# Kernel tuning notes

Measured on AMD Instinct MI355X. Metric: run time of the kernel, lower is better.

## Reference

```python
import jax, jax.numpy as jnp
import numpy as np

NUM_GRAPHS = 512
NODES_PER_GRAPH = 200  # == N_rois
EDGES_PER_GRAPH = 3200  # avg degree 16
N_ROIS = 200
HIDDEN = 64
OUT = 2


def setup_inputs() -> dict:
    key = jax.random.key(0)
    ks = jax.random.split(key, 7)
    N = NUM_GRAPHS * NODES_PER_GRAPH
    E = NUM_GRAPHS * EDGES_PER_GRAPH
    x = jax.random.normal(ks[0], (N, N_ROIS), dtype=jnp.float32)
    # edges sampled within each graph's node block
    base = jnp.repeat(jnp.arange(NUM_GRAPHS, dtype=jnp.int64) * NODES_PER_GRAPH, EDGES_PER_GRAPH)
    local = jax.random.randint(ks[1], (2, E), 0, NODES_PER_GRAPH, dtype=jnp.int64)
    edge_index = local + base[None, :]
    batch = jnp.arange(N, dtype=jnp.int64) // NODES_PER_GRAPH
    conv_w = jax.random.normal(ks[2], (N_ROIS, HIDDEN), dtype=jnp.float32) * 0.1
    conv_b = jax.random.normal(ks[3], (HIDDEN,), dtype=jnp.float32) * 0.1
    lin_w = jax.random.normal(ks[4], (HIDDEN, OUT), dtype=jnp.float32) * 0.1
    lin_b = jax.random.normal(ks[5], (OUT,), dtype=jnp.float32) * 0.1
    return {"x": x, "edge_index": edge_index, "batch": batch,
            "conv_w": conv_w, "conv_b": conv_b, "lin_w": lin_w, "lin_b": lin_b}


def reference(x, edge_index, batch, conv_w, conv_b, lin_w, lin_b):
    N = x.shape[0]
    # GCNConv: linear transform first (N_rois -> hidden), then normalized aggregation
    h = x @ conv_w  # [N, H]
    loops = jnp.arange(N, dtype=edge_index.dtype)
    src = jnp.concatenate([edge_index[0], loops])  # add self-loops (PyG default)
    dst = jnp.concatenate([edge_index[1], loops])
    deg = jax.ops.segment_sum(jnp.ones_like(dst, dtype=h.dtype), dst, num_segments=N)
    dinv = jnp.where(deg > 0, jax.lax.rsqrt(deg), jnp.zeros_like(deg))
    norm = dinv[src] * dinv[dst]  # D^-1/2 (A+I) D^-1/2 edge weights
    agg = jax.ops.segment_sum(h[src] * norm[:, None], dst, num_segments=N) + conv_b
    hr = jax.nn.relu(agg)
    x_pool = jax.ops.segment_max(hr, batch, num_segments=NUM_GRAPHS)  # [G, H]
    out = x_pool @ lin_w + lin_b  # [G, OUT]
    return out, x_pool
```

## Files before the change

kernel.cpp:

```cpp
#include <hip/hip_runtime.h>

#define NUM_GRAPHS 512
#define NPG 200
#define EPG 3200
#define NROIS 200
#define HID 64
#define OUTC 2
#define KPAD 224
#define THREADS 512
#define APITCH 232
#define HPITCH 232

typedef short v8s __attribute__((ext_vector_type(8)));
typedef float v4f __attribute__((ext_vector_type(4)));

__device__ __forceinline__ unsigned bf16_rne(float f) {
  unsigned u = __float_as_uint(f);
  return (u + 0x7fffu + ((u >> 16) & 1u)) >> 16;
}

__global__ void prep_w(const float* __restrict__ cw, short* __restrict__ ws) {
  int idx = blockIdx.x * 256 + threadIdx.x;
  if (idx >= HID * KPAD) return;
  int ch = idx / KPAD, k = idx - ch * KPAD;
  float f = (k < NROIS) ? cw[k * HID + ch] : 0.f;
  unsigned hi = bf16_rne(f);
  float lo = f - __uint_as_float(hi << 16);
  ws[ch * KPAD + k] = (short)hi;
  ws[HID * KPAD + ch * KPAD + k] = (short)(__float_as_uint(lo) >> 16);
}

struct __align__(16) Smem {
  unsigned char adj[208 * APITCH];
  unsigned short hpT[HID * HPITCH];
  float dinv[NPG];
  int cnt[NPG];
  int pool[HID];
};

__global__ __launch_bounds__(THREADS, 4)
void gcn_fused(const float* __restrict__ x,
               const int* __restrict__ ei,
               const short* __restrict__ wT,
               const float* __restrict__ cw,
               const float* __restrict__ cb,
               const float* __restrict__ lw,
               const float* __restrict__ lb,
               float* __restrict__ out,
               int Etot, int useWs) {
  __shared__ Smem s;
  const int g = blockIdx.x;
  const int tid = threadIdx.x;
  const int base = g * NPG;
  const int ebase = g * EPG;
  const int lane = tid & 63;
  const int w = __builtin_amdgcn_readfirstlane(tid >> 6);
  const int ml = tid & 15;
  const int q  = (tid >> 4) & 3;

  {
    uint4* z = (uint4*)&s;
    const uint4 z4 = {0u, 0u, 0u, 0u};
    #pragma unroll
    for (int i = 0; i < 10; ++i) {
      int idx = tid + i * THREADS;
      if (idx < (208 * APITCH + HID * HPITCH * 2) / 16) z[idx] = z4;
    }
    if (tid < NPG) s.cnt[tid] = 0;
    if (tid < HID) s.pool[tid] = 0;
  }
  __syncthreads();

  int esrc[7], edst[7];
  #pragma unroll
  for (int r = 0; r < 7; ++r) {
    int e = tid + r * THREADS;
    esrc[r] = -1; edst[r] = 0;
    if (e < EPG) {
      esrc[r] = ei[ebase + e] - base;
      edst[r] = ei[Etot + ebase + e] - base;
      atomicAdd(&s.cnt[edst[r]], 1);
    }
  }
  __syncthreads();

  if (w == 0) {
    if (lane < 50) {
      #pragma unroll
      for (int t = 0; t < 4; ++t) {
        int i = 4 * lane + t;
        s.dinv[i] = rsqrtf((float)(s.cnt[i] + 1));
      }
    }
  }

  {
    unsigned* adjW = (unsigned*)s.adj;
    #pragma unroll
    for (int r = 0; r < 7; ++r) {
      if (esrc[r] >= 0) {
        int idx = edst[r] * APITCH + esrc[r];
        atomicAdd(&adjW[idx >> 2], 1u << ((idx & 3) * 8));
      }
    }
    if (tid < NPG) {
      int idx = tid * APITCH + tid;
      atomicAdd(&adjW[idx >> 2], 1u << ((idx & 3) * 8));
    }
  }
  __syncthreads();

  {
    int mts[2];
    mts[0] = w;
    mts[1] = (w < 5) ? 8 + w : -1;

    v4f acc[2][4];
    #pragma unroll
    for (int a = 0; a < 2; ++a)
      #pragma unroll
      for (int b = 0; b < 4; ++b)
        acc[a][b] = (v4f){0.f, 0.f, 0.f, 0.f};

    for (int kt = 0; kt < 7; ++kt) {
      const int k0 = kt * 32 + q * 8;

      v8s bhi[4], blo[4];
      if (useWs) {
        #pragma unroll
        for (int nt = 0; nt < 4; ++nt) {
          const int ch = nt * 16 + ml;
          bhi[nt] = *(const v8s*)(wT + ch * KPAD + k0);
          blo[nt] = *(const v8s*)(wT + HID * KPAD + ch * KPAD + k0);
        }
      } else {
        const bool kok = (k0 < NROIS);
        #pragma unroll
        for (int nt = 0; nt < 4; ++nt) {
          #pragma unroll
          for (int i = 0; i < 8; ++i) {
            float f = kok ? cw[(k0 + i) * HID + nt * 16 + ml] : 0.f;
            unsigned hb = bf16_rne(f);
            float lo = f - __uint_as_float(hb << 16);
            bhi[nt][i] = (short)hb;
            blo[nt][i] = (short)(__float_as_uint(lo) >> 16);
          }
        }
      }

      #pragma unroll
      for (int mi = 0; mi < 2; ++mi) {
        if (mts[mi] >= 0) {
          const int row = mts[mi] * 16 + ml;
          v8s ahi, alo;
          if (k0 < NROIS && row < NPG) {
            const float* px = x + (size_t)(base + row) * NROIS + k0;
            const float4 f0 = *(const float4*)px;
            const float4 f1 = *(const float4*)(px + 4);
            const float ff[8] = {f0.x, f0.y, f0.z, f0.w, f1.x, f1.y, f1.z, f1.w};
            #pragma unroll
            for (int i = 0; i < 8; ++i) {
              unsigned u = __float_as_uint(ff[i]);
              unsigned hb = u >> 16;
              float lo = ff[i] - __uint_as_float(hb << 16);
              ahi[i] = (short)hb;
              alo[i] = (short)(__float_as_uint(lo) >> 16);
            }
          } else {
            #pragma unroll
            for (int i = 0; i < 8; ++i) { ahi[i] = 0; alo[i] = 0; }
          }
          #pragma unroll
          for (int nt = 0; nt < 4; ++nt) {
            acc[mi][nt] = __builtin_amdgcn_mfma_f32_16x16x32_bf16(ahi, blo[nt], acc[mi][nt], 0, 0, 0);
            acc[mi][nt] = __builtin_amdgcn_mfma_f32_16x16x32_bf16(alo, bhi[nt], acc[mi][nt], 0, 0, 0);
            acc[mi][nt] = __builtin_amdgcn_mfma_f32_16x16x32_bf16(ahi, bhi[nt], acc[mi][nt], 0, 0, 0);
          }
        }
      }
    }

    #pragma unroll
    for (int mi = 0; mi < 2; ++mi) {
      if (mts[mi] >= 0) {
        #pragma unroll
        for (int r = 0; r < 4; ++r) {
          const int row = mts[mi] * 16 + q * 4 + r;
          if (row < NPG) {
            const float dv = s.dinv[row];
            #pragma unroll
            for (int nt = 0; nt < 4; ++nt)
              s.hpT[(nt * 16 + ml) * HPITCH + row] =
                  (unsigned short)bf16_rne(dv * acc[mi][nt][r]);
          }
        }
      }
    }
  }
  __syncthreads();

  {
    int mts[2];
    mts[0] = w;
    mts[1] = (w < 5) ? 8 + w : -1;

    v4f acc2[2][4];
    #pragma unroll
    for (int a = 0; a < 2; ++a)
      #pragma unroll
      for (int b = 0; b < 4; ++b)
        acc2[a][b] = (v4f){0.f, 0.f, 0.f, 0.f};

    for (int kt = 0; kt < 7; ++kt) {
      const int k0 = kt * 32 + q * 8;

      v8s bf[4];
      #pragma unroll
      for (int nt = 0; nt < 4; ++nt)
        bf[nt] = *(const v8s*)&s.hpT[(nt * 16 + ml) * HPITCH + k0];

      #pragma unroll
      for (int mi = 0; mi < 2; ++mi) {
        if (mts[mi] >= 0) {
          const int row = mts[mi] * 16 + ml;
          const uint2 dd = *(const uint2*)&s.adj[row * APITCH + k0];
          v8s af;
          #pragma unroll
          for (int i = 0; i < 4; ++i) {
            af[i]     = (short)(__float_as_uint((float)((dd.x >> (8 * i)) & 0xffu)) >> 16);
            af[i + 4] = (short)(__float_as_uint((float)((dd.y >> (8 * i)) & 0xffu)) >> 16);
          }
          #pragma unroll
          for (int nt = 0; nt < 4; ++nt)
            acc2[mi][nt] = __builtin_amdgcn_mfma_f32_16x16x32_bf16(af, bf[nt], acc2[mi][nt], 0, 0, 0);
        }
      }
    }

    float cbv[4];
    #pragma unroll
    for (int nt = 0; nt < 4; ++nt) cbv[nt] = cb[nt * 16 + ml];
    float mx[4] = {0.f, 0.f, 0.f, 0.f};
    #pragma unroll
    for (int mi = 0; mi < 2; ++mi) {
      if (mts[mi] >= 0) {
        #pragma unroll
        for (int r = 0; r < 4; ++r) {
          const int row = mts[mi] * 16 + q * 4 + r;
          if (row < NPG) {
            const float dv = s.dinv[row];
            #pragma unroll
            for (int nt = 0; nt < 4; ++nt) {
              float v = fmaxf(fmaf(dv, acc2[mi][nt][r], cbv[nt]), 0.f);
              mx[nt] = fmaxf(mx[nt], v);
            }
          }
        }
      }
    }
    #pragma unroll
    for (int nt = 0; nt < 4; ++nt) {
      mx[nt] = fmaxf(mx[nt], __shfl_xor(mx[nt], 16));
      mx[nt] = fmaxf(mx[nt], __shfl_xor(mx[nt], 32));
    }
    if (q == 0 && (lane >> 5) == 0) {
      #pragma unroll
      for (int nt = 0; nt < 4; ++nt)
        atomicMax(&s.pool[nt * 16 + ml], __float_as_int(mx[nt]));
    }
  }
  __syncthreads();

  if (tid < HID) {
    const float xp = __int_as_float(s.pool[tid]);
    out[NUM_GRAPHS * OUTC + g * HID + tid] = xp;
    float p0 = xp * lw[tid * 2 + 0];
    float p1 = xp * lw[tid * 2 + 1];
    #pragma unroll
    for (int off = 32; off > 0; off >>= 1) {
      p0 += __shfl_down(p0, off);
      p1 += __shfl_down(p1, off);
    }
    if (tid == 0) {
      out[g * OUTC + 0] = p0 + lb[0];
      out[g * OUTC + 1] = p1 + lb[1];
    }
  }
}

extern "C" void kernel_launch(void* const* d_in, const int* in_sizes, int n_in,
                              void* d_out, int out_size, void* d_ws, size_t ws_size,
                              hipStream_t stream) {
  const float* x  = (const float*)d_in[0];
  const int*   ei = (const int*)d_in[1];
  const float* cw = (const float*)d_in[3];
  const float* cb = (const float*)d_in[4];
  const float* lw = (const float*)d_in[5];
  const float* lb = (const float*)d_in[6];
  const int Etot = in_sizes[1] / 2;

  const size_t wsNeeded = (size_t)2 * HID * KPAD * sizeof(short);
  const int useWs = (ws_size >= wsNeeded) ? 1 : 0;
  if (useWs) {
    prep_w<<<(HID * KPAD + 255) / 256, 256, 0, stream>>>(cw, (short*)d_ws);
  }
  gcn_fused<<<NUM_GRAPHS, THREADS, 0, stream>>>(x, ei, (const short*)d_ws, cw,
                                                cb, lw, lb, (float*)d_out, Etot, useWs);
}
```

Before: 164.0 us.

## Split fused GCN into separate dense GEMM kernel and per-graph aggregation kernel

Moves the x @ conv_w product out of the per-graph fused kernel into its own GEMM kernel over 64-node tiles. That kernel stages x as split bf16 hi/lo in LDS and reads a pre-swizzled weight image laid out in MFMA lane order. Its bf16 output goes to a global workspace in transposed layout, and the aggregation kernel scales it by dinv while loading. The aim is higher occupancy and better load balance for the GEMM stage, which in the fused kernel ran at one 512-thread block per graph. In exchange it adds an extra global round trip of the hidden features (about 6.5 MB) and another kernel launch. The old fused path is kept as a fallback for when the workspace is too small.

```diff
diff --git a/kernel.cpp b/kernel.cpp
--- a/kernel.cpp
+++ b/kernel.cpp
@@ -6,10 +6,11 @@
 #define NROIS 200
 #define HID 64
 #define OUTC 2
-#define KPAD 224
-#define THREADS 512
+#define NT (NUM_GRAPHS * NPG)
 #define APITCH 232
 #define HPITCH 232
+#define WIMG_ELEMS (7 * 4 * 2 * 64 * 8)
+#define WS_NEEDED ((size_t)WIMG_ELEMS * 2 + (size_t)HID * NT * 2)
 
 typedef short v8s __attribute__((ext_vector_type(8)));
 typedef float v4f __attribute__((ext_vector_type(4)));
@@ -19,36 +20,115 @@
   return (u + 0x7fffu + ((u >> 16) & 1u)) >> 16;
 }
 
-__global__ void prep_w(const float* __restrict__ cw, short* __restrict__ ws) {
+__global__ void prep_wimg(const float* __restrict__ cw, unsigned short* __restrict__ wimg) {
   int idx = blockIdx.x * 256 + threadIdx.x;
-  if (idx >= HID * KPAD) return;
-  int ch = idx / KPAD, k = idx - ch * KPAD;
+  if (idx >= WIMG_ELEMS) return;
+  int i    = idx & 7;
+  int lane = (idx >> 3) & 63;
+  int hl   = (idx >> 9) & 1;
+  int nt   = (idx >> 10) & 3;
+  int kt   = idx >> 12;
+  int k  = kt * 32 + (lane >> 4) * 8 + i;
+  int ch = nt * 16 + (lane & 15);
   float f = (k < NROIS) ? cw[k * HID + ch] : 0.f;
   unsigned hi = bf16_rne(f);
   float lo = f - __uint_as_float(hi << 16);
-  ws[ch * KPAD + k] = (short)hi;
-  ws[HID * KPAD + ch * KPAD + k] = (short)(__float_as_uint(lo) >> 16);
+  wimg[idx] = hl ? (unsigned short)(__float_as_uint(lo) >> 16) : (unsigned short)hi;
 }
 
-struct __align__(16) Smem {
+struct __align__(16) Smem1 {
+  unsigned short xhi[64 * HPITCH];
+  unsigned short xlo[64 * HPITCH];
+};
+
+__global__ __launch_bounds__(256, 2)
+void gcn_gemm1(const float* __restrict__ x,
+               const unsigned short* __restrict__ wimg,
+               unsigned short* __restrict__ hpT) {
+  __shared__ Smem1 s;
+  const int tid = threadIdx.x;
+  const int blk = blockIdx.x;
+  const int lane = tid & 63;
+  const int w = __builtin_amdgcn_readfirstlane(tid >> 6);
+  const int ml = tid & 15;
+  const int q  = (tid >> 4) & 3;
+
+  #pragma unroll
+  for (int t = 0; t < 13; ++t) {
+    int i = tid + t * 256;
+    if (i < 3200) {
+      int node = i / 50;
+      int kc = (i - node * 50) * 4;
+      const float4 v = *(const float4*)(x + (size_t)(blk * 64 + node) * NROIS + kc);
+      const float ff[4] = {v.x, v.y, v.z, v.w};
+      unsigned hh[4], ll[4];
+      #pragma unroll
+      for (int e = 0; e < 4; ++e) {
+        unsigned u = __float_as_uint(ff[e]);
+        hh[e] = u >> 16;
+        float lo = ff[e] - __uint_as_float(hh[e] << 16);
+        ll[e] = __float_as_uint(lo) >> 16;
+      }
+      uint2 ph = {hh[0] | (hh[1] << 16), hh[2] | (hh[3] << 16)};
+      uint2 pl = {ll[0] | (ll[1] << 16), ll[2] | (ll[3] << 16)};
+      *(uint2*)&s.xhi[node * HPITCH + kc] = ph;
+      *(uint2*)&s.xlo[node * HPITCH + kc] = pl;
+    }
+  }
+  for (int i = tid; i < 64 * 32; i += 256) {
+    int node = i >> 5, c = 200 + (i & 31);
+    s.xhi[node * HPITCH + c] = 0;
+    s.xlo[node * HPITCH + c] = 0;
+  }
+  __syncthreads();
+
+  v4f acc[4];
+  #pragma unroll
+  for (int nt = 0; nt < 4; ++nt) acc[nt] = (v4f){0.f, 0.f, 0.f, 0.f};
+
+  for (int kt = 0; kt < 7; ++kt) {
+    const int k0 = kt * 32 + q * 8;
+    const v8s xh = *(const v8s*)&s.xhi[(w * 16 + ml) * HPITCH + k0];
+    const v8s xl = *(const v8s*)&s.xlo[(w * 16 + ml) * HPITCH + k0];
+    #pragma unroll
+    for (int nt = 0; nt < 4; ++nt) {
+      const unsigned short* pw = wimg + (size_t)(((kt * 4 + nt) * 2) * 64 + lane) * 8;
+      const v8s whi = *(const v8s*)pw;
+      const v8s wlo = *(const v8s*)(pw + 64 * 8);
+      acc[nt] = __builtin_amdgcn_mfma_f32_16x16x32_bf16(whi, xl, acc[nt], 0, 0, 0);
+      acc[nt] = __builtin_amdgcn_mfma_f32_16x16x32_bf16(wlo, xh, acc[nt], 0, 0, 0);
+      acc[nt] = __builtin_amdgcn_mfma_f32_16x16x32_bf16(whi, xh, acc[nt], 0, 0, 0);
+    }
+  }
+
+  const int gnode = blk * 64 + w * 16 + ml;
+  #pragma unroll
+  for (int nt = 0; nt < 4; ++nt) {
+    #pragma unroll
+    for (int r = 0; r < 4; ++r) {
+      const int ch = nt * 16 + q * 4 + r;
+      hpT[(size_t)ch * NT + gnode] = (unsigned short)bf16_rne(acc[nt][r]);
+    }
+  }
+}
+
+struct __align__(16) Smem2 {
   unsigned char adj[208 * APITCH];
-  unsigned short hpT[HID * HPITCH];
+  unsigned short hpTl[HID * HPITCH];
   float dinv[NPG];
   int cnt[NPG];
   int pool[HID];
 };
 
-__global__ __launch_bounds__(THREADS, 4)
-void gcn_fused(const float* __restrict__ x,
-               const int* __restrict__ ei,
-               const short* __restrict__ wT,
-               const float* __restrict__ cw,
-               const float* __restrict__ cb,
-               const float* __restrict__ lw,
-               const float* __restrict__ lb,
-               float* __restrict__ out,
-               int Etot, int useWs) {
-  __shared__ Smem s;
+__global__ __launch_bounds__(512, 4)
+void gcn_agg(const int* __restrict__ ei,
+             const unsigned short* __restrict__ hpT,
+             const float* __restrict__ cb,
+             const float* __restrict__ lw,
+             const float* __restrict__ lb,
+             float* __restrict__ out,
+             int Etot) {
+  __shared__ Smem2 s;
   const int g = blockIdx.x;
   const int tid = threadIdx.x;
   const int base = g * NPG;
@@ -63,7 +143,7 @@
     const uint4 z4 = {0u, 0u, 0u, 0u};
     #pragma unroll
     for (int i = 0; i < 10; ++i) {
-      int idx = tid + i * THREADS;
+      int idx = tid + i * 512;
       if (idx < (208 * APITCH + HID * HPITCH * 2) / 16) z[idx] = z4;
     }
     if (tid < NPG) s.cnt[tid] = 0;
@@ -74,7 +154,7 @@
   int esrc[7], edst[7];
   #pragma unroll
   for (int r = 0; r < 7; ++r) {
-    int e = tid + r * THREADS;
+    int e = tid + r * 512;
     esrc[r] = -1; edst[r] = 0;
     if (e < EPG) {
       esrc[r] = ei[ebase + e] - base;
@@ -84,15 +164,8 @@
   }
   __syncthreads();
 
-  if (w == 0) {
-    if (lane < 50) {
-      #pragma unroll
-      for (int t = 0; t < 4; ++t) {
-        int i = 4 * lane + t;
-        s.dinv[i] = rsqrtf((float)(s.cnt[i] + 1));
-      }
-    }
-  }
+  if (tid < NPG) s.dinv[tid] = rsqrtf((float)(s.cnt[tid] + 1));
+  __syncthreads();
 
   {
     unsigned* adjW = (unsigned*)s.adj;
@@ -108,6 +181,19 @@
       atomicAdd(&adjW[idx >> 2], 1u << ((idx & 3) * 8));
     }
   }
+
+  #pragma unroll
+  for (int t = 0; t < 13; ++t) {
+    int i = tid + t * 512;
+    if (i < HID * 100) {
+      int ch = i / 100;
+      int c2 = (i - ch * 100) * 2;
+      unsigned v = *(const unsigned*)(hpT + (size_t)ch * NT + base + c2);
+      float f0 = __uint_as_float(v << 16)         * s.dinv[c2];
+      float f1 = __uint_as_float(v & 0xffff0000u) * s.dinv[c2 + 1];
+      *(unsigned*)&s.hpTl[ch * HPITCH + c2] = bf16_rne(f0) | (bf16_rne(f1) << 16);
+    }
+  }
   __syncthreads();
 
   {
@@ -115,6 +201,165 @@
     mts[0] = w;
     mts[1] = (w < 5) ? 8 + w : -1;
 
+    v4f acc2[2][4];
+    #pragma unroll
+    for (int a = 0; a < 2; ++a)
+      #pragma unroll
+      for (int b = 0; b < 4; ++b)
+        acc2[a][b] = (v4f){0.f, 0.f, 0.f, 0.f};
+
+    for (int kt = 0; kt < 7; ++kt) {
+      const int k0 = kt * 32 + q * 8;
+
+      v8s bf[4];
+      #pragma unroll
+      for (int nt = 0; nt < 4; ++nt)
+        bf[nt] = *(const v8s*)&s.hpTl[(nt * 16 + ml) * HPITCH + k0];
+
+      #pragma unroll
+      for (int mi = 0; mi < 2; ++mi) {
+        if (mts[mi] >= 0) {
+          const int row = mts[mi] * 16 + ml;
+          const uint2 dd = *(const uint2*)&s.adj[row * APITCH + k0];
+          v8s af;
+          #pragma unroll
+          for (int i = 0; i < 4; ++i) {
+            af[i]     = (short)(__float_as_uint((float)((dd.x >> (8 * i)) & 0xffu)) >> 16);
+            af[i + 4] = (short)(__float_as_uint((float)((dd.y >> (8 * i)) & 0xffu)) >> 16);
+          }
+          #pragma unroll
+          for (int nt = 0; nt < 4; ++nt)
+            acc2[mi][nt] = __builtin_amdgcn_mfma_f32_16x16x32_bf16(af, bf[nt], acc2[mi][nt], 0, 0, 0);
+        }
+      }
+    }
+
+    float cbv[4];
+    #pragma unroll
+    for (int nt = 0; nt < 4; ++nt) cbv[nt] = cb[nt * 16 + ml];
+    float mx[4] = {0.f, 0.f, 0.f, 0.f};
+    #pragma unroll
+    for (int mi = 0; mi < 2; ++mi) {
+      if (mts[mi] >= 0) {
+        #pragma unroll
+        for (int r = 0; r < 4; ++r) {
+          const int row = mts[mi] * 16 + q * 4 + r;
+          if (row < NPG) {
+            const float dv = s.dinv[row];
+            #pragma unroll
+            for (int nt = 0; nt < 4; ++nt) {
+              float v = fmaxf(fmaf(dv, acc2[mi][nt][r], cbv[nt]), 0.f);
+              mx[nt] = fmaxf(mx[nt], v);
+            }
+          }
+        }
+      }
+    }
+    #pragma unroll
+    for (int nt = 0; nt < 4; ++nt) {
+      mx[nt] = fmaxf(mx[nt], __shfl_xor(mx[nt], 16));
+      mx[nt] = fmaxf(mx[nt], __shfl_xor(mx[nt], 32));
+    }
+    if (q == 0 && (lane >> 5) == 0) {
+      #pragma unroll
+      for (int nt = 0; nt < 4; ++nt)
+        atomicMax(&s.pool[nt * 16 + ml], __float_as_int(mx[nt]));
+    }
+  }
+  __syncthreads();
+
+  if (tid < HID) {
+    const float xp = __int_as_float(s.pool[tid]);
+    out[NUM_GRAPHS * OUTC + g * HID + tid] = xp;
+    float p0 = xp * lw[tid * 2 + 0];
+    float p1 = xp * lw[tid * 2 + 1];
+    #pragma unroll
+    for (int off = 32; off > 0; off >>= 1) {
+      p0 += __shfl_down(p0, off);
+      p1 += __shfl_down(p1, off);
+    }
+    if (tid == 0) {
+      out[g * OUTC + 0] = p0 + lb[0];
+      out[g * OUTC + 1] = p1 + lb[1];
+    }
+  }
+}
+
+struct __align__(16) SmemF {
+  unsigned char adj[208 * APITCH];
+  unsigned short hpT[HID * HPITCH];
+  float dinv[NPG];
+  int cnt[NPG];
+  int pool[HID];
+};
+
+__global__ __launch_bounds__(512, 4)
+void gcn_fused_fb(const float* __restrict__ x,
+                  const int* __restrict__ ei,
+                  const float* __restrict__ cw,
+                  const float* __restrict__ cb,
+                  const float* __restrict__ lw,
+                  const float* __restrict__ lb,
+                  float* __restrict__ out,
+                  int Etot) {
+  __shared__ SmemF s;
+  const int g = blockIdx.x;
+  const int tid = threadIdx.x;
+  const int base = g * NPG;
+  const int ebase = g * EPG;
+  const int lane = tid & 63;
+  const int w = __builtin_amdgcn_readfirstlane(tid >> 6);
+  const int ml = tid & 15;
+  const int q  = (tid >> 4) & 3;
+
+  {
+    uint4* z = (uint4*)&s;
+    const uint4 z4 = {0u, 0u, 0u, 0u};
+    #pragma unroll
+    for (int i = 0; i < 10; ++i) {
+      int idx = tid + i * 512;
+      if (idx < (208 * APITCH + HID * HPITCH * 2) / 16) z[idx] = z4;
+    }
+    if (tid < NPG) s.cnt[tid] = 0;
+    if (tid < HID) s.pool[tid] = 0;
+  }
+  __syncthreads();
+
+  int esrc[7], edst[7];
+  #pragma unroll
+  for (int r = 0; r < 7; ++r) {
+    int e = tid + r * 512;
+    esrc[r] = -1; edst[r] = 0;
+    if (e < EPG) {
+      esrc[r] = ei[ebase + e] - base;
+      edst[r] = ei[Etot + ebase + e] - base;
+      atomicAdd(&s.cnt[edst[r]], 1);
+    }
+  }
+  __syncthreads();
+
+  if (tid < NPG) s.dinv[tid] = rsqrtf((float)(s.cnt[tid] + 1));
+
+  {
+    unsigned* adjW = (unsigned*)s.adj;
+    #pragma unroll
+    for (int r = 0; r < 7; ++r) {
+      if (esrc[r] >= 0) {
+        int idx = edst[r] * APITCH + esrc[r];
+        atomicAdd(&adjW[idx >> 2], 1u << ((idx & 3) * 8));
+      }
+    }
+    if (tid < NPG) {
+      int idx = tid * APITCH + tid;
+      atomicAdd(&adjW[idx >> 2], 1u << ((idx & 3) * 8));
+    }
+  }
+  __syncthreads();
+
+  {
+    int mts[2];
+    mts[0] = w;
+    mts[1] = (w < 5) ? 8 + w : -1;
     v4f acc[2][4];
     #pragma unroll
     for (int a = 0; a < 2; ++a)
@@ -124,36 +369,25 @@
 
     for (int kt = 0; kt < 7; ++kt) {
       const int k0 = kt * 32 + q * 8;
-
+      const bool kok = (k0 < NROIS);
       v8s bhi[4], blo[4];
-      if (useWs) {
+      #pragma unroll
+      for (int nt = 0; nt < 4; ++nt) {
         #pragma unroll
-        for (int nt = 0; nt < 4; ++nt) {
-          const int ch = nt * 16 + ml;
-          bhi[nt] = *(const v8s*)(wT + ch * KPAD + k0);
-          blo[nt] = *(const v8s*)(wT + HID * KPAD + ch * KPAD + k0);
-        }
-      } else {
-        const bool kok = (k0 < NROIS);
-        #pragma unroll
-        for (int nt = 0; nt < 4; ++nt) {
-          #pragma unroll
-          for (int i = 0; i < 8; ++i) {
-            float f = kok ? cw[(k0 + i) * HID + nt * 16 + ml] : 0.f;
-            unsigned hb = bf16_rne(f);
-            float lo = f - __uint_as_float(hb << 16);
-            bhi[nt][i] = (short)hb;
-            blo[nt][i] = (short)(__float_as_uint(lo) >> 16);
-          }
-        }
-      }
-
+        for (int i = 0; i < 8; ++i) {
+          float f = kok ? cw[(k0 + i) * HID + nt * 16 + ml] : 0.f;
+          unsigned hb = bf16_rne(f);
+          float lo = f - __uint_as_float(hb << 16);
+          bhi[nt][i] = (short)hb;
+          blo[nt][i] = (short)(__float_as_uint(lo) >> 16);
+        }
+      }
       #pragma unroll
       for (int mi = 0; mi < 2; ++mi) {
         if (mts[mi] >= 0) {
           const int row = mts[mi] * 16 + ml;
           v8s ahi, alo;
-          if (k0 < NROIS && row < NPG) {
+          if (kok && row < NPG) {
             const float* px = x + (size_t)(base + row) * NROIS + k0;
             const float4 f0 = *(const float4*)px;
             const float4 f1 = *(const float4*)(px + 4);
@@ -179,7 +413,6 @@
         }
       }
     }
-
     #pragma unroll
     for (int mi = 0; mi < 2; ++mi) {
       if (mts[mi] >= 0) {
@@ -203,7 +436,6 @@
     int mts[2];
     mts[0] = w;
     mts[1] = (w < 5) ? 8 + w : -1;
-
     v4f acc2[2][4];
     #pragma unroll
     for (int a = 0; a < 2; ++a)
@@ -213,12 +445,10 @@
 
     for (int kt = 0; kt < 7; ++kt) {
       const int k0 = kt * 32 + q * 8;
-
       v8s bf[4];
       #pragma unroll
       for (int nt = 0; nt < 4; ++nt)
         bf[nt] = *(const v8s*)&s.hpT[(nt * 16 + ml) * HPITCH + k0];
-
       #pragma unroll
       for (int mi = 0; mi < 2; ++mi) {
         if (mts[mi] >= 0) {
@@ -299,11 +529,14 @@
   const float* lb = (const float*)d_in[6];
   const int Etot = in_sizes[1] / 2;
 
-  const size_t wsNeeded = (size_t)2 * HID * KPAD * sizeof(short);
-  const int useWs = (ws_size >= wsNeeded) ? 1 : 0;
-  if (useWs) {
-    prep_w<<<(HID * KPAD + 255) / 256, 256, 0, stream>>>(cw, (short*)d_ws);
-  }
-  gcn_fused<<<NUM_GRAPHS, THREADS, 0, stream>>>(x, ei, (const short*)d_ws, cw,
-                                                cb, lw, lb, (float*)d_out, Etot, useWs);
+  if (ws_size >= WS_NEEDED) {
+    unsigned short* wimg = (unsigned short*)d_ws;
+    unsigned short* hpT  = wimg + WIMG_ELEMS;
+    prep_wimg<<<(WIMG_ELEMS + 255) / 256, 256, 0, stream>>>(cw, wimg);
+    gcn_gemm1<<<NT / 64, 256, 0, stream>>>(x, wimg, hpT);
+    gcn_agg<<<NUM_GRAPHS, 512, 0, stream>>>(ei, hpT, cb, lw, lb, (float*)d_out, Etot);
+  } else {
+    gcn_fused_fb<<<NUM_GRAPHS, 512, 0, stream>>>(x, ei, cw, cb, lw, lb,
+                                                 (float*)d_out, Etot);
+  }
 }
```

After: 167.8 us. 1.02x slower.
